# Performance work log

Measured on AMD Instinct MI355X. Metric: run time of the kernel, lower is better.

The kernel has to match this reference:

```python
import jax, jax.numpy as jnp
import numpy as np

N = 100000      # nodes
E = 1600000     # edges
F_IN = 64       # num_features
H = 64          # hidden_channels
NG = 64         # graphs in batch
ALPHA = 0.5


def _lin_init(key, fan_in, fan_out):
    kw, kb = jax.random.split(key)
    bound = 1.0 / np.sqrt(fan_in)
    w = jax.random.uniform(kw, (fan_in, fan_out), jnp.float32, -bound, bound)
    b = jax.random.uniform(kb, (fan_out,), jnp.float32, -bound, bound)
    return w, b


def setup_inputs() -> dict:
    key = jax.random.key(0)
    ks = jax.random.split(key, 12)
    x = jax.random.normal(ks[0], (N, F_IN), dtype=jnp.float32)
    edge_index = jax.random.randint(ks[1], (2, E), 0, N, dtype=jnp.int32)
    batch = jnp.sort(jax.random.randint(ks[2], (N,), 0, NG, dtype=jnp.int32))
    w1s, b1s = _lin_init(ks[3], F_IN, H)
    w1d, b1d = _lin_init(ks[4], F_IN, H)
    w2s, b2s = _lin_init(ks[5], H, H)
    w2d, b2d = _lin_init(ks[6], H, H)
    w3s, b3s = _lin_init(ks[7], H, H)
    w3d, b3d = _lin_init(ks[8], H, H)
    wl1, bl1 = _lin_init(ks[9], H, 5)
    wl2, bl2 = _lin_init(ks[10], 5, 1)
    return dict(x=x, edge_index=edge_index, batch=batch,
                w1s=w1s, b1s=b1s, w1d=w1d, b1d=b1d,
                w2s=w2s, b2s=b2s, w2d=w2d, b2d=b2d,
                w3s=w3s, b3s=b3s, w3d=w3d, b3d=b3d,
                wl1=wl1, bl1=bl1, wl2=wl2, bl2=bl2)


def _dir_gcn_conv(x, row, col, ws, bs, wd, bd):
    # directional norm: D_out^{-1/2} A D_in^{-1/2} (and same recipe for A^T)
    ones = jnp.ones((row.shape[0],), x.dtype)
    deg_out = jax.ops.segment_sum(ones, row, num_segments=N)  # row-sums of A
    deg_in = jax.ops.segment_sum(ones, col, num_segments=N)   # col-sums of A
    r_out = jnp.where(deg_out > 0, deg_out ** -0.5, 0.0)
    r_in = jnp.where(deg_in > 0, deg_in ** -0.5, 0.0)
    norm = r_out[row] * r_in[col]  # per-edge weight; identical for A and A^T norms
    msg = norm[:, None] * x[col]                       # [E, F]
    adj_x = jax.ops.segment_sum(msg, row, num_segments=N)
    msg_t = norm[:, None] * x[row]
    adj_t_x = jax.ops.segment_sum(msg_t, col, num_segments=N)
    return ALPHA * (adj_x @ ws + bs) + (1.0 - ALPHA) * (adj_t_x @ wd + bd)


def reference(x, edge_index, batch,
              w1s, b1s, w1d, b1d,
              w2s, b2s, w2d, b2d,
              w3s, b3s, w3d, b3d,
              wl1, bl1, wl2, bl2):
    row, col = edge_index[0], edge_index[1]
    h = jax.nn.relu(_dir_gcn_conv(x, row, col, w1s, b1s, w1d, b1d))
    h = jax.nn.relu(_dir_gcn_conv(h, row, col, w2s, b2s, w2d, b2d))
    h = jax.nn.relu(_dir_gcn_conv(h, row, col, w3s, b3s, w3d, b3d))
    g = jax.ops.segment_max(h, batch, num_segments=NG)  # global max pool [NG, H]
    g = jax.nn.relu(g @ wl1 + bl1)
    return g @ wl2 + bl2  # [NG, 1]
```

## Files before the change

kernel.cpp:

```cpp
#include <hip/hip_runtime.h>

#define N_NODES 100000
#define N_EDGES 1600000
#define EPAD    (N_EDGES + N_NODES)
#define HDIM    64
#define NGRAPH  64
#define BW      256
#define NB      391
#define NBLK    256
#define CHUNK   ((N_EDGES + NBLK - 1) / NBLK)
#define MTILES  (N_NODES / 16)

typedef _Float16 h16;
typedef _Float16 h16x4 __attribute__((ext_vector_type(4)));
typedef _Float16 h16x8 __attribute__((ext_vector_type(8)));
typedef float    f32x4 __attribute__((ext_vector_type(4)));

__global__ __launch_bounds__(512) void bucket_count(const int* __restrict__ ei,
                                                    int* __restrict__ cntTabA,
                                                    int* __restrict__ cntTabT) {
    __shared__ int cA[NB], cT[NB];
    const int tid = threadIdx.x;
    for (int i = tid; i < NB; i += 512) { cA[i] = 0; cT[i] = 0; }
    __syncthreads();
    const int e0 = blockIdx.x * CHUNK, e1 = min(e0 + CHUNK, N_EDGES);
    for (int e = e0 + tid; e < e1; e += 512) {
        int r = ei[e];
        int c = ei[N_EDGES + e];
        atomicAdd(&cA[r >> 8], 1);
        atomicAdd(&cT[c >> 8], 1);
    }
    __syncthreads();
    for (int b = tid; b < NB; b += 512) {
        cntTabA[b * NBLK + blockIdx.x] = cA[b];
        cntTabT[b * NBLK + blockIdx.x] = cT[b];
    }
}

__global__ __launch_bounds__(256) void chunk_scan(int* __restrict__ cntTabA,
                                                  int* __restrict__ cntTabT,
                                                  int* __restrict__ tot) {
    __shared__ int s[256];
    const int b = blockIdx.x, d = blockIdx.y, tid = threadIdx.x;
    int* tab = d ? cntTabT : cntTabA;
    int v = tab[b * NBLK + tid];
    s[tid] = v;
    __syncthreads();
    for (int off = 1; off < 256; off <<= 1) {
        int t = (tid >= off) ? s[tid - off] : 0;
        __syncthreads();
        s[tid] += t;
        __syncthreads();
    }
    tab[b * NBLK + tid] = s[tid] - v;
    if (tid == 255) tot[d * 512 + b] = s[255];
}

__global__ __launch_bounds__(512) void start_scan(const int* __restrict__ tot,
                                                  int* __restrict__ bktStartA,
                                                  int* __restrict__ bktStartT) {
    __shared__ int s[512];
    const int tid = threadIdx.x;
    int v = (tid < NB) ? tot[tid] : 0;
    s[tid] = v;
    __syncthreads();
    for (int off = 1; off < 512; off <<= 1) {
        int t = (tid >= off) ? s[tid - off] : 0;
        __syncthreads();
        s[tid] += t;
        __syncthreads();
    }
    if (tid < NB) bktStartA[tid] = s[tid] - v;
    if (tid == 0) bktStartA[NB] = N_EDGES;
    __syncthreads();
    int v2 = (tid < NB) ? tot[512 + tid] : 0;
    s[tid] = v2;
    __syncthreads();
    for (int off = 1; off < 512; off <<= 1) {
        int t = (tid >= off) ? s[tid - off] : 0;
        __syncthreads();
        s[tid] += t;
        __syncthreads();
    }
    if (tid < NB) bktStartT[tid] = s[tid] - v2;
    if (tid == 0) bktStartT[NB] = N_EDGES;
}

__global__ __launch_bounds__(512) void bucketize_write(const int* __restrict__ ei,
                                                       const int* __restrict__ cntTabA,
                                                       const int* __restrict__ cntTabT,
                                                       const int* __restrict__ bktStartA,
                                                       const int* __restrict__ bktStartT,
                                                       int2* __restrict__ bktA,
                                                       int2* __restrict__ bktT) {
    __shared__ int bA[NB], bT[NB];
    const int tid = threadIdx.x;
    for (int i = tid; i < NB; i += 512) {
        bA[i] = bktStartA[i] + cntTabA[i * NBLK + blockIdx.x];
        bT[i] = bktStartT[i] + cntTabT[i * NBLK + blockIdx.x];
    }
    __syncthreads();
    const int e0 = blockIdx.x * CHUNK, e1 = min(e0 + CHUNK, N_EDGES);
    for (int e = e0 + tid; e < e1; e += 512) {
        int r = ei[e];
        int c = ei[N_EDGES + e];
        int pA = atomicAdd(&bA[r >> 8], 1);
        bktA[pA] = make_int2(r, c);
        int pT = atomicAdd(&bT[c >> 8], 1);
        bktT[pT] = make_int2(c, r);
    }
}

__global__ __launch_bounds__(256) void bucket_deg(const int* __restrict__ bktStartA,
                                                  const int* __restrict__ bktStartT,
                                                  const int2* __restrict__ bktA,
                                                  const int2* __restrict__ bktT,
                                                  int* __restrict__ deg_out,
                                                  int* __restrict__ deg_in,
                                                  float* __restrict__ r_out,
                                                  float* __restrict__ r_in,
                                                  int* __restrict__ padSum) {
    __shared__ int c[BW];
    __shared__ int red[256];
    const int b = blockIdx.x, d = blockIdx.y, tid = threadIdx.x;
    const int* bs = d ? bktStartT : bktStartA;
    const int2* bkt = d ? bktT : bktA;
    int* deg = d ? deg_in : deg_out;
    float* rr = d ? r_in : r_out;
    const int node0 = b * BW;
    c[tid] = 0;
    __syncthreads();
    const int i0 = bs[b], i1 = bs[b + 1];
    for (int i = i0 + tid; i < i1; i += 256) atomicAdd(&c[bkt[i].x - node0], 1);
    __syncthreads();
    int n = node0 + tid, dg = c[tid], pad = 0;
    if (n < N_NODES) {
        deg[n] = dg;
        rr[n] = dg > 0 ? rsqrtf((float)dg) : 0.0f;
        pad = dg + (dg & 1);
    }
    red[tid] = pad;
    __syncthreads();
    for (int off = 128; off > 0; off >>= 1) {
        if (tid < off) red[tid] += red[tid + off];
        __syncthreads();
    }
    if (tid == 0) padSum[d * 512 + b] = red[0];
}

__global__ __launch_bounds__(512) void pad_scan(const int* __restrict__ padSum,
                                                int* __restrict__ padStart) {
    __shared__ int s[512];
    const int tid = threadIdx.x;
    int v = (tid < NB) ? padSum[tid] : 0;
    s[tid] = v;
    __syncthreads();
    for (int off = 1; off < 512; off <<= 1) {
        int t = (tid >= off) ? s[tid - off] : 0;
        __syncthreads();
        s[tid] += t;
        __syncthreads();
    }
    if (tid < NB) padStart[tid] = s[tid] - v;
    __syncthreads();
    int v2 = (tid < NB) ? padSum[512 + tid] : 0;
    s[tid] = v2;
    __syncthreads();
    for (int off = 1; off < 512; off <<= 1) {
        int t = (tid >= off) ? s[tid - off] : 0;
        __syncthreads();
        s[tid] += t;
        __syncthreads();
    }
    if (tid < NB) padStart[512 + tid] = s[tid] - v2;
}

__global__ __launch_bounds__(256) void node_ptr(const int* __restrict__ padStart,
                                                const int* __restrict__ deg_out,
                                                const int* __restrict__ deg_in,
                                                int* __restrict__ rowptrP,
                                                int* __restrict__ colptrP) {
    __shared__ int s[256];
    const int b = blockIdx.x, d = blockIdx.y, tid = threadIdx.x;
    const int* deg = d ? deg_in : deg_out;
    int* ptr = d ? colptrP : rowptrP;
    int n = b * BW + tid;
    int pad = 0;
    if (n < N_NODES) { int dg = deg[n]; pad = dg + (dg & 1); }
    s[tid] = pad;
    __syncthreads();
    for (int off = 1; off < 256; off <<= 1) {
        int t = (tid >= off) ? s[tid - off] : 0;
        __syncthreads();
        s[tid] += t;
        __syncthreads();
    }
    if (n < N_NODES) ptr[n] = padStart[d * 512 + b] + s[tid] - pad;
}

__global__ __launch_bounds__(512) void bucket_scatter(
        const int* __restrict__ rowptrP, const int* __restrict__ colptrP,
        const float* __restrict__ r_out, const float* __restrict__ r_in,
        const int* __restrict__ bktStartA, const int* __restrict__ bktStartT,
        const int2* __restrict__ bktA, const int2* __restrict__ bktT,
        int2* __restrict__ recA, int2* __restrict__ recT) {
    __shared__ int cur[BW];
    __shared__ float rwt[BW];
    const int b = blockIdx.x, d = blockIdx.y, tid = threadIdx.x;
    const int* ptr = d ? colptrP : rowptrP;
    const float* rt = d ? r_in : r_out;
    const float* rs = d ? r_out : r_in;
    const int* bs = d ? bktStartT : bktStartA;
    const int2* bkt = d ? bktT : bktA;
    int2* rec = d ? recT : recA;
    const int node0 = b * BW;
    if (tid < BW) {
        int n = node0 + tid;
        cur[tid] = (n < N_NODES) ? ptr[n] : 0;
        rwt[tid] = (n < N_NODES) ? rt[n] : 0.0f;
    }
    __syncthreads();
    const int i0 = bs[b], i1 = bs[b + 1];
    for (int i = i0 + tid; i < i1; i += 512) {
        int2 e = bkt[i];
        float w = rwt[e.x - node0] * rs[e.y];
        int p = atomicAdd(&cur[e.x - node0], 1);
        rec[p] = make_int2(e.y << 7, __float_as_int(w));
    }
}

__global__ __launch_bounds__(256) void cast_kernel(const float4* __restrict__ x,
                                                   h16x4* __restrict__ xh) {
    int i = blockIdx.x * 256 + threadIdx.x;
    if (i < N_NODES * 16) {
        float4 v = x[i];
        h16x4 o;
        o.x = (h16)v.x; o.y = (h16)v.y; o.z = (h16)v.z; o.w = (h16)v.w;
        xh[i] = o;
    }
}

__global__ __launch_bounds__(256) void wprep_kernel(
        const float* __restrict__ w1s, const float* __restrict__ w1d,
        const float* __restrict__ w2s, const float* __restrict__ w2d,
        const float* __restrict__ w3s, const float* __restrict__ w3d,
        const float* __restrict__ b1s, const float* __restrict__ b1d,
        const float* __restrict__ b2s, const float* __restrict__ b2d,
        const float* __restrict__ b3s, const float* __restrict__ b3d,
        h16* __restrict__ WT, float* __restrict__ bc) {
    const int l = blockIdx.y;
    const float* ws = l == 0 ? w1s : l == 1 ? w2s : w3s;
    const float* wd = l == 0 ? w1d : l == 1 ? w2d : w3d;
    int e = blockIdx.x * 256 + threadIdx.x;
    if (e < 8192) {
        int f = e >> 7, k = e & 127;
        float v = (k < 64) ? ws[k * 64 + f] : wd[(k - 64) * 64 + f];
        WT[l * 8192 + f * 128 + k] = (h16)(0.5f * v);
    }
    if (blockIdx.x == 0 && threadIdx.x < 64) {
        const float* bs = l == 0 ? b1s : l == 1 ? b2s : b3s;
        const float* bd = l == 0 ? b1d : l == 1 ? b2d : b3d;
        bc[l * 64 + threadIdx.x] = 0.5f * (bs[threadIdx.x] + bd[threadIdx.x]);
    }
}

__device__ __forceinline__ void fma4h(float4& a, float w, h16x4 f) {
    a.x = fmaf(w, (float)f.x, a.x);
    a.y = fmaf(w, (float)f.y, a.y);
    a.z = fmaf(w, (float)f.z, a.z);
    a.w = fmaf(w, (float)f.w, a.w);
}

__device__ __forceinline__ float4 red_s(float4 v) {
    v.x += __shfl_xor(v.x, 16); v.y += __shfl_xor(v.y, 16);
    v.z += __shfl_xor(v.z, 16); v.w += __shfl_xor(v.w, 16);
    v.x += __shfl_xor(v.x, 32); v.y += __shfl_xor(v.y, 32);
    v.z += __shfl_xor(v.z, 32); v.w += __shfl_xor(v.w, 32);
    return v;
}

__device__ __forceinline__ h16x4 ld_h4(const char* __restrict__ p) {
    return *(const h16x4*)p;
}

__device__ __forceinline__ float4 agg_dir(const char* __restrict__ hb,
                                          const int2* __restrict__ rec,
                                          int start, int deg, int q, int s, int sh) {
    float4 a0 = {0.f,0.f,0.f,0.f}, a1 = {0.f,0.f,0.f,0.f};
    float4 a2 = {0.f,0.f,0.f,0.f}, a3 = {0.f,0.f,0.f,0.f};
    const int4* rec4 = (const int4*)(rec + start);
    const int qb = q * 8;
    int k = 0;
    for (; k + 16 <= deg; k += 16) {
        int4 p0 = rec4[(k >> 1) + s];
        int4 p1 = rec4[(k >> 1) + 4 + s];
        h16x4 f0 = ld_h4(hb + (p0.x << sh) + qb);
        h16x4 f1 = ld_h4(hb + (p0.z << sh) + qb);
        h16x4 f2 = ld_h4(hb + (p1.x << sh) + qb);
        h16x4 f3 = ld_h4(hb + (p1.z << sh) + qb);
        fma4h(a0, __int_as_float(p0.y), f0);
        fma4h(a1, __int_as_float(p0.w), f1);
        fma4h(a2, __int_as_float(p1.y), f2);
        fma4h(a3, __int_as_float(p1.w), f3);
    }
    if (k + 8 <= deg) {
        int4 p = rec4[(k >> 1) + s];
        h16x4 f0 = ld_h4(hb + (p.x << sh) + qb);
        h16x4 f1 = ld_h4(hb + (p.z << sh) + qb);
        fma4h(a0, __int_as_float(p.y), f0);
        fma4h(a1, __int_as_float(p.w), f1);
        k += 8;
    }
    int r = deg - k;
    if (2 * s < r) {
        int4 p = rec4[(k >> 1) + s];
        h16x4 f0 = ld_h4(hb + (p.x << sh) + qb);
        fma4h(a2, __int_as_float(p.y), f0);
        if (2 * s + 1 < r) {
            h16x4 f1 = ld_h4(hb + (p.z << sh) + qb);
            fma4h(a3, __int_as_float(p.w), f1);
        }
    }
    a0.x += a1.x; a0.y += a1.y; a0.z += a1.z; a0.w += a1.w;
    a2.x += a3.x; a2.y += a3.y; a2.z += a3.z; a2.w += a3.w;
    a0.x += a2.x; a0.y += a2.y; a0.z += a2.z; a0.w += a2.w;
    return red_s(a0);
}

__global__ __launch_bounds__(256) void agg_kernel(
        const char* __restrict__ h_in, char* __restrict__ acc_out, int sh,
        const int* __restrict__ rowptrP, const int* __restrict__ deg_out,
        const int2* __restrict__ recA,
        const int* __restrict__ colptrP, const int* __restrict__ deg_in,
        const int2* __restrict__ recT) {
    const int tid  = threadIdx.x;
    const int wid  = (blockIdx.x << 2) + (tid >> 6);
    const int lane = tid & 63;
    const int node = wid >> 1;
    const int dir  = wid & 1;
    const int q = lane & 15;
    const int s = lane >> 4;

    const int* ptr = dir ? colptrP : rowptrP;
    const int* deg = dir ? deg_in : deg_out;
    const int2* rec = dir ? recT : recA;

    float4 a = agg_dir(h_in, rec, ptr[node], deg[node], q, s, sh);
    if (s == 0) {
        h16x4 pk;
        pk.x = (h16)a.x; pk.y = (h16)a.y; pk.z = (h16)a.z; pk.w = (h16)a.w;
        *(h16x4*)(acc_out + (size_t)node * 256 + dir * 128 + q * 8) = pk;
    }
}

__global__ __launch_bounds__(256) void gemm_kernel(char* __restrict__ acc,
                                                   const h16* __restrict__ WT,
                                                   const float* __restrict__ bc) {
    const int lane = threadIdx.x & 63;
    const int wid = (blockIdx.x * 256 + threadIdx.x) >> 6;
    const int nW = gridDim.x * 4;
    const int m = lane & 15, t = lane >> 4;

    h16x8 bfrag[4][4];
    float bb[4];
#pragma unroll
    for (int nt = 0; nt < 4; nt++) {
        bb[nt] = bc[nt * 16 + m];
#pragma unroll
        for (int kk = 0; kk < 4; kk++)
            bfrag[nt][kk] = *(const h16x8*)(WT + (nt * 16 + m) * 128 + kk * 32 + t * 8);
    }

    for (int tile = wid; tile < MTILES; tile += nW) {
        char* arow = acc + (size_t)tile * 16 * 256;
        h16x8 afrag[4];
#pragma unroll
        for (int kk = 0; kk < 4; kk++)
            afrag[kk] = *(const h16x8*)(arow + m * 256 + kk * 64 + t * 16);
#pragma unroll
        for (int nt = 0; nt < 4; nt++) {
            f32x4 c = {0.f, 0.f, 0.f, 0.f};
#pragma unroll
            for (int kk = 0; kk < 4; kk++)
                c = __builtin_amdgcn_mfma_f32_16x16x32_f16(afrag[kk], bfrag[nt][kk], c, 0, 0, 0);
#pragma unroll
            for (int r = 0; r < 4; r++) {
                float o = fmaxf(c[r] + bb[nt], 0.0f);
                *(h16*)(arow + (t * 4 + r) * 256 + (nt * 16 + m) * 2) = (h16)o;
            }
        }
    }
}

__global__ __launch_bounds__(256) void pool_kernel(const h16* __restrict__ h,
                                                   const int* __restrict__ batch,
                                                   unsigned* __restrict__ g) {
    int t = blockIdx.x * 256 + threadIdx.x;
    const int ngroups = N_NODES / 16;
    if (t >= ngroups * 64) return;
    int f = t & 63;
    int n0 = (t >> 6) * 16;
    int curg = batch[n0];
    float m = 0.0f;
    for (int n = n0; n < n0 + 16; n++) {
        int b = batch[n];
        if (b != curg) {
            atomicMax(&g[curg * HDIM + f], __float_as_uint(m));
            curg = b;
            m = 0.0f;
        }
        m = fmaxf(m, (float)h[(size_t)n * 128 + f]);
    }
    atomicMax(&g[curg * HDIM + f], __float_as_uint(m));
}

__global__ __launch_bounds__(64) void mlp_kernel(const unsigned* __restrict__ g,
                                                 const float* __restrict__ wl1,
                                                 const float* __restrict__ bl1,
                                                 const float* __restrict__ wl2,
                                                 const float* __restrict__ bl2,
                                                 float* __restrict__ out) {
    int t = threadIdx.x;
    float gv[HDIM];
#pragma unroll
    for (int k = 0; k < HDIM; k++) gv[k] = __uint_as_float(g[t * HDIM + k]);
    float o = bl2[0];
#pragma unroll
    for (int j = 0; j < 5; j++) {
        float hj = bl1[j];
#pragma unroll
        for (int k = 0; k < HDIM; k++) hj += gv[k] * wl1[k * 5 + j];
        hj = fmaxf(hj, 0.0f);
        o += hj * wl2[j];
    }
    out[t] = o;
}

extern "C" void kernel_launch(void* const* d_in, const int* in_sizes, int n_in,
                              void* d_out, int out_size, void* d_ws, size_t ws_size,
                              hipStream_t stream) {
    const float* x   = (const float*)d_in[0];
    const int*   ei  = (const int*)d_in[1];
    const int*   bat = (const int*)d_in[2];
    const float* w1s = (const float*)d_in[3];
    const float* b1s = (const float*)d_in[4];
    const float* w1d = (const float*)d_in[5];
    const float* b1d = (const float*)d_in[6];
    const float* w2s = (const float*)d_in[7];
    const float* b2s = (const float*)d_in[8];
    const float* w2d = (const float*)d_in[9];
    const float* b2d = (const float*)d_in[10];
    const float* w3s = (const float*)d_in[11];
    const float* b3s = (const float*)d_in[12];
    const float* w3d = (const float*)d_in[13];
    const float* b3d = (const float*)d_in[14];
    const float* wl1 = (const float*)d_in[15];
    const float* bl1 = (const float*)d_in[16];
    const float* wl2 = (const float*)d_in[17];
    const float* bl2 = (const float*)d_in[18];
    float* out = (float*)d_out;

    char* p = (char*)d_ws;
    int*   deg_out = (int*)p;              p += N_NODES * 4;
    int*   deg_in  = (int*)p;              p += N_NODES * 4;
    int*   rowptrP = (int*)p;              p += N_NODES * 4;
    int*   colptrP = (int*)p;              p += N_NODES * 4;
    float* r_out   = (float*)p;            p += N_NODES * 4;
    float* r_in    = (float*)p;            p += N_NODES * 4;
    int*   cntTabA = (int*)p;              p += (size_t)NB * NBLK * 4;
    int*   cntTabT = (int*)p;              p += (size_t)NB * NBLK * 4;
    int*   totTab  = (int*)p;              p += 1024 * 4;
    int*   bktStartA = (int*)p;            p += 512 * 4;
    int*   bktStartT = (int*)p;            p += 512 * 4;
    int*   padSum  = (int*)p;              p += 1024 * 4;
    int*   padStart = (int*)p;             p += 1024 * 4;
    int2*  recA    = (int2*)p;             p += (size_t)EPAD * 8;
    int2*  recT    = (int2*)p;             p += (size_t)EPAD * 8;
    char*  bufP    = p;
    int2*  bktA    = (int2*)p;
    int2*  bktT    = (int2*)(p + (size_t)N_EDGES * 8);
    p += 2 * (size_t)N_EDGES * 8;
    char*  bufQ    = p;
    h16*   xh      = (h16*)p;
    p += 2 * (size_t)N_EDGES * 8;
    unsigned* g    = (unsigned*)p;         p += NGRAPH * HDIM * 4;
    h16*   WT      = (h16*)p;              p += 3 * 8192 * 2;
    float* bc      = (float*)p;            p += 3 * 64 * 4;

    hipMemsetAsync(g, 0, NGRAPH * HDIM * 4, stream);

    cast_kernel<<<(N_NODES * 16 + 255) / 256, 256, 0, stream>>>(
        (const float4*)x, (h16x4*)xh);
    dim3 gw(32, 3);
    wprep_kernel<<<gw, 256, 0, stream>>>(w1s, w1d, w2s, w2d, w3s, w3d,
                                         b1s, b1d, b2s, b2d, b3s, b3d, WT, bc);

    bucket_count<<<NBLK, 512, 0, stream>>>(ei, cntTabA, cntTabT);
    dim3 gb2(NB, 2);
    chunk_scan<<<gb2, 256, 0, stream>>>(cntTabA, cntTabT, totTab);
    start_scan<<<1, 512, 0, stream>>>(totTab, bktStartA, bktStartT);
    bucketize_write<<<NBLK, 512, 0, stream>>>(ei, cntTabA, cntTabT,
                                              bktStartA, bktStartT, bktA, bktT);

    dim3 gb(NB, 2);
    bucket_deg<<<gb, 256, 0, stream>>>(bktStartA, bktStartT, bktA, bktT,
                                       deg_out, deg_in, r_out, r_in, padSum);
    pad_scan<<<1, 512, 0, stream>>>(padSum, padStart);
    node_ptr<<<gb, 256, 0, stream>>>(padStart, deg_out, deg_in, rowptrP, colptrP);
    bucket_scatter<<<gb, 512, 0, stream>>>(
        rowptrP, colptrP, r_out, r_in, bktStartA, bktStartT, bktA, bktT, recA, recT);

    const int agrid = N_NODES * 2 / 4;
    agg_kernel<<<agrid, 256, 0, stream>>>((const char*)xh, bufP, 0,
                                          rowptrP, deg_out, recA, colptrP, deg_in, recT);
    gemm_kernel<<<256, 256, 0, stream>>>(bufP, WT, bc);
    agg_kernel<<<agrid, 256, 0, stream>>>(bufP, bufQ, 1,
                                          rowptrP, deg_out, recA, colptrP, deg_in, recT);
    gemm_kernel<<<256, 256, 0, stream>>>(bufQ, WT + 8192, bc + 64);
    agg_kernel<<<agrid, 256, 0, stream>>>(bufQ, bufP, 1,
                                          rowptrP, deg_out, recA, colptrP, deg_in, recT);
    gemm_kernel<<<256, 256, 0, stream>>>(bufP, WT + 16384, bc + 128);

    const int pool_threads = (N_NODES / 16) * 64;
    pool_kernel<<<(pool_threads + 255) / 256, 256, 0, stream>>>((const h16*)bufP, bat, g);

    mlp_kernel<<<1, 64, 0, stream>>>(g, wl1, bl1, wl2, bl2, out);
}
```

Before: 493.2 us.

## Fuse degree/pointer kernels, pool into final GEMM, and pool-buffer zeroing into cast

Merges bucket_deg, pad_scan and node_ptr into one kernel. The global pad scan is removed by giving each bucket a slack region of up to BW extra slots (EPAD grows), so each node pointer is derived from the bucket start plus a local scan. The global max pool moves into the last GEMM's epilogue, using wave shuffles and atomicMax, and the memset of g moves into cast_kernel. Together these drop four launches and one reread of the final activations, at the cost of a larger padded record buffer and extra atomics in the GEMM epilogue.

```diff
diff --git a/kernel.cpp b/kernel.cpp
--- a/kernel.cpp
+++ b/kernel.cpp
@@ -2,7 +2,7 @@
 
 #define N_NODES 100000
 #define N_EDGES 1600000
-#define EPAD    (N_EDGES + N_NODES)
+#define EPAD    (N_EDGES + NB * BW)
 #define HDIM    64
 #define NGRAPH  64
 #define BW      256
@@ -111,82 +111,32 @@
     }
 }
 
-__global__ __launch_bounds__(256) void bucket_deg(const int* __restrict__ bktStartA,
-                                                  const int* __restrict__ bktStartT,
-                                                  const int2* __restrict__ bktA,
-                                                  const int2* __restrict__ bktT,
-                                                  int* __restrict__ deg_out,
-                                                  int* __restrict__ deg_in,
-                                                  float* __restrict__ r_out,
-                                                  float* __restrict__ r_in,
-                                                  int* __restrict__ padSum) {
+__global__ __launch_bounds__(256) void bucket_deg_ptr(
+        const int* __restrict__ bktStartA, const int* __restrict__ bktStartT,
+        const int2* __restrict__ bktA, const int2* __restrict__ bktT,
+        int* __restrict__ deg_out, int* __restrict__ deg_in,
+        float* __restrict__ r_out, float* __restrict__ r_in,
+        int* __restrict__ rowptrP, int* __restrict__ colptrP) {
     __shared__ int c[BW];
-    __shared__ int red[256];
+    __shared__ int s[256];
     const int b = blockIdx.x, d = blockIdx.y, tid = threadIdx.x;
     const int* bs = d ? bktStartT : bktStartA;
     const int2* bkt = d ? bktT : bktA;
     int* deg = d ? deg_in : deg_out;
     float* rr = d ? r_in : r_out;
+    int* ptr = d ? colptrP : rowptrP;
     const int node0 = b * BW;
     c[tid] = 0;
     __syncthreads();
     const int i0 = bs[b], i1 = bs[b + 1];
     for (int i = i0 + tid; i < i1; i += 256) atomicAdd(&c[bkt[i].x - node0], 1);
     __syncthreads();
-    int n = node0 + tid, dg = c[tid], pad = 0;
+    int n = node0 + tid, dg = c[tid];
+    int pad = dg + (dg & 1);
     if (n < N_NODES) {
         deg[n] = dg;
         rr[n] = dg > 0 ? rsqrtf((float)dg) : 0.0f;
-        pad = dg + (dg & 1);
-    }
-    red[tid] = pad;
-    __syncthreads();
-    for (int off = 128; off > 0; off >>= 1) {
-        if (tid < off) red[tid] += red[tid + off];
-        __syncthreads();
-    }
-    if (tid == 0) padSum[d * 512 + b] = red[0];
-}
-
-__global__ __launch_bounds__(512) void pad_scan(const int* __restrict__ padSum,
-                                                int* __restrict__ padStart) {
-    __shared__ int s[512];
-    const int tid = threadIdx.x;
-    int v = (tid < NB) ? padSum[tid] : 0;
-    s[tid] = v;
-    __syncthreads();
-    for (int off = 1; off < 512; off <<= 1) {
-        int t = (tid >= off) ? s[tid - off] : 0;
-        __syncthreads();
-        s[tid] += t;
-        __syncthreads();
-    }
-    if (tid < NB) padStart[tid] = s[tid] - v;
-    __syncthreads();
-    int v2 = (tid < NB) ? padSum[512 + tid] : 0;
-    s[tid] = v2;
-    __syncthreads();
-    for (int off = 1; off < 512; off <<= 1) {
-        int t = (tid >= off) ? s[tid - off] : 0;
-        __syncthreads();
-        s[tid] += t;
-        __syncthreads();
-    }
-    if (tid < NB) padStart[512 + tid] = s[tid] - v2;
-}
-
-__global__ __launch_bounds__(256) void node_ptr(const int* __restrict__ padStart,
-                                                const int* __restrict__ deg_out,
-                                                const int* __restrict__ deg_in,
-                                                int* __restrict__ rowptrP,
-                                                int* __restrict__ colptrP) {
-    __shared__ int s[256];
-    const int b = blockIdx.x, d = blockIdx.y, tid = threadIdx.x;
-    const int* deg = d ? deg_in : deg_out;
-    int* ptr = d ? colptrP : rowptrP;
-    int n = b * BW + tid;
-    int pad = 0;
-    if (n < N_NODES) { int dg = deg[n]; pad = dg + (dg & 1); }
+    } else pad = 0;
     s[tid] = pad;
     __syncthreads();
     for (int off = 1; off < 256; off <<= 1) {
@@ -195,7 +145,7 @@
         s[tid] += t;
         __syncthreads();
     }
-    if (n < N_NODES) ptr[n] = padStart[d * 512 + b] + s[tid] - pad;
+    if (n < N_NODES) ptr[n] = i0 + b * BW + (s[tid] - pad);
 }
 
 __global__ __launch_bounds__(512) void bucket_scatter(
@@ -230,7 +180,11 @@
 }
 
 __global__ __launch_bounds__(256) void cast_kernel(const float4* __restrict__ x,
-                                                   h16x4* __restrict__ xh) {
+                                                   h16x4* __restrict__ xh,
+                                                   unsigned* __restrict__ g) {
+    if (blockIdx.x == 0) {
+        for (int j = threadIdx.x; j < NGRAPH * HDIM; j += 256) g[j] = 0u;
+    }
     int i = blockIdx.x * 256 + threadIdx.x;
     if (i < N_NODES * 16) {
         float4 v = x[i];
@@ -355,7 +309,10 @@
 
 __global__ __launch_bounds__(256) void gemm_kernel(char* __restrict__ acc,
                                                    const h16* __restrict__ WT,
-                                                   const float* __restrict__ bc) {
+                                                   const float* __restrict__ bc,
+                                                   const int* __restrict__ batch,
+                                                   unsigned* __restrict__ g,
+                                                   int do_pool) {
     const int lane = threadIdx.x & 63;
     const int wid = (blockIdx.x * 256 + threadIdx.x) >> 6;
     const int nW = gridDim.x * 4;
@@ -373,6 +330,9 @@
 
     for (int tile = wid; tile < MTILES; tile += nW) {
         char* arow = acc + (size_t)tile * 16 * 256;
+        const int node0 = tile * 16;
+        int b0 = 0, b15 = 0;
+        if (do_pool) { b0 = batch[node0]; b15 = batch[node0 + 15]; }
         h16x8 afrag[4];
 #pragma unroll
         for (int kk = 0; kk < 4; kk++)
@@ -383,35 +343,28 @@
 #pragma unroll
             for (int kk = 0; kk < 4; kk++)
                 c = __builtin_amdgcn_mfma_f32_16x16x32_f16(afrag[kk], bfrag[nt][kk], c, 0, 0, 0);
+            float ov[4];
 #pragma unroll
             for (int r = 0; r < 4; r++) {
-                float o = fmaxf(c[r] + bb[nt], 0.0f);
-                *(h16*)(arow + (t * 4 + r) * 256 + (nt * 16 + m) * 2) = (h16)o;
+                ov[r] = fmaxf(c[r] + bb[nt], 0.0f);
+                *(h16*)(arow + (t * 4 + r) * 256 + (nt * 16 + m) * 2) = (h16)ov[r];
+            }
+            if (do_pool) {
+                if (b0 == b15) {
+                    float mx = fmaxf(fmaxf(ov[0], ov[1]), fmaxf(ov[2], ov[3]));
+                    mx = fmaxf(mx, __shfl_xor(mx, 16));
+                    mx = fmaxf(mx, __shfl_xor(mx, 32));
+                    if (t == 0)
+                        atomicMax(&g[b0 * HDIM + nt * 16 + m], __float_as_uint(mx));
+                } else {
+#pragma unroll
+                    for (int r = 0; r < 4; r++)
+                        atomicMax(&g[batch[node0 + t * 4 + r] * HDIM + nt * 16 + m],
+                                  __float_as_uint(ov[r]));
+                }
             }
         }
     }
-}
-
-__global__ __launch_bounds__(256) void pool_kernel(const h16* __restrict__ h,
-                                                   const int* __restrict__ batch,
-                                                   unsigned* __restrict__ g) {
-    int t = blockIdx.x * 256 + threadIdx.x;
-    const int ngroups = N_NODES / 16;
-    if (t >= ngroups * 64) return;
-    int f = t & 63;
-    int n0 = (t >> 6) * 16;
-    int curg = batch[n0];
-    float m = 0.0f;
-    for (int n = n0; n < n0 + 16; n++) {
-        int b = batch[n];
-        if (b != curg) {
-            atomicMax(&g[curg * HDIM + f], __float_as_uint(m));
-            curg = b;
-            m = 0.0f;
-        }
-        m = fmaxf(m, (float)h[(size_t)n * 128 + f]);
-    }
-    atomicMax(&g[curg * HDIM + f], __float_as_uint(m));
 }
 
 __global__ __launch_bounds__(64) void mlp_kernel(const unsigned* __restrict__ g,
@@ -472,8 +425,6 @@
     int*   totTab  = (int*)p;              p += 1024 * 4;
     int*   bktStartA = (int*)p;            p += 512 * 4;
     int*   bktStartT = (int*)p;            p += 512 * 4;
-    int*   padSum  = (int*)p;              p += 1024 * 4;
-    int*   padStart = (int*)p;             p += 1024 * 4;
     int2*  recA    = (int2*)p;             p += (size_t)EPAD * 8;
     int2*  recT    = (int2*)p;             p += (size_t)EPAD * 8;
     char*  bufP    = p;
@@ -487,10 +438,8 @@
     h16*   WT      = (h16*)p;              p += 3 * 8192 * 2;
     float* bc      = (float*)p;            p += 3 * 64 * 4;
 
-    hipMemsetAsync(g, 0, NGRAPH * HDIM * 4, stream);
-
     cast_kernel<<<(N_NODES * 16 + 255) / 256, 256, 0, stream>>>(
-        (const float4*)x, (h16x4*)xh);
+        (const float4*)x, (h16x4*)xh, g);
     dim3 gw(32, 3);
     wprep_kernel<<<gw, 256, 0, stream>>>(w1s, w1d, w2s, w2d, w3s, w3d,
                                          b1s, b1d, b2s, b2d, b3s, b3d, WT, bc);
@@ -503,26 +452,22 @@
                                               bktStartA, bktStartT, bktA, bktT);
 
     dim3 gb(NB, 2);
-    bucket_deg<<<gb, 256, 0, stream>>>(bktStartA, bktStartT, bktA, bktT,
-                                       deg_out, deg_in, r_out, r_in, padSum);
-    pad_scan<<<1, 512, 0, stream>>>(padSum, padStart);
-    node_ptr<<<gb, 256, 0, stream>>>(padStart, deg_out, deg_in, rowptrP, colptrP);
+    bucket_deg_ptr<<<gb, 256, 0, stream>>>(bktStartA, bktStartT, bktA, bktT,
+                                           deg_out, deg_in, r_out, r_in,
+                                           rowptrP, colptrP);
     bucket_scatter<<<gb, 512, 0, stream>>>(
         rowptrP, colptrP, r_out, r_in, bktStartA, bktStartT, bktA, bktT, recA, recT);
 
     const int agrid = N_NODES * 2 / 4;
     agg_kernel<<<agrid, 256, 0, stream>>>((const char*)xh, bufP, 0,
                                           rowptrP, deg_out, recA, colptrP, deg_in, recT);
-    gemm_kernel<<<256, 256, 0, stream>>>(bufP, WT, bc);
+    gemm_kernel<<<256, 256, 0, stream>>>(bufP, WT, bc, bat, g, 0);
     agg_kernel<<<agrid, 256, 0, stream>>>(bufP, bufQ, 1,
                                           rowptrP, deg_out, recA, colptrP, deg_in, recT);
-    gemm_kernel<<<256, 256, 0, stream>>>(bufQ, WT + 8192, bc + 64);
+    gemm_kernel<<<256, 256, 0, stream>>>(bufQ, WT + 8192, bc + 64, bat, g, 0);
     agg_kernel<<<agrid, 256, 0, stream>>>(bufQ, bufP, 1,
                                           rowptrP, deg_out, recA, colptrP, deg_in, recT);
-    gemm_kernel<<<256, 256, 0, stream>>>(bufP, WT + 16384, bc + 128);
-
-    const int pool_threads = (N_NODES / 16) * 64;
-    pool_kernel<<<(pool_threads + 255) / 256, 256, 0, stream>>>((const h16*)bufP, bat, g);
+    gemm_kernel<<<256, 256, 0, stream>>>(bufP, WT + 16384, bc + 128, bat, g, 1);
 
     mlp_kernel<<<1, 64, 0, stream>>>(g, wl1, bl1, wl2, bl2, out);
 }
```

Measured after the change: 489.0 us. About the same (-0.9%).
